# Kernel tuning notes

Measured on AMD Instinct MI355X. Metric: run time of the kernel, lower is better.

Reference implementation:

```python
import jax, jax.numpy as jnp
import numpy as np


def _l2norm(t, axis=-1, eps=1e-12):
    # matches torch F.normalize: x / max(||x||, eps)
    n = jnp.sqrt(jnp.sum(t * t, axis=axis, keepdims=True))
    return t / jnp.maximum(n, eps)


def setup_inputs() -> dict:
    key = jax.random.key(0)
    ks = jax.random.split(key, 5)
    B, N, C, H = 16, 4096, 768, 12
    x = jax.random.normal(ks[0], (B, N, C), dtype=jnp.float32)
    Wqkv = jax.random.normal(ks[1], (C, 3 * C), dtype=jnp.float32) * (C ** -0.5)
    bqkv = jax.random.normal(ks[2], (3 * C,), dtype=jnp.float32) * 0.02
    Wproj = jax.random.normal(ks[3], (C, C), dtype=jnp.float32) * (C ** -0.5)
    bproj = jax.random.normal(ks[4], (C,), dtype=jnp.float32) * 0.02
    temperature = jnp.ones((H, 1, 1), dtype=jnp.float32)
    return {"x": x, "Wqkv": Wqkv, "bqkv": bqkv, "Wproj": Wproj,
            "bproj": bproj, "temperature": temperature}


def reference(x, Wqkv, bqkv, Wproj, bproj, temperature):
    B, N, C = x.shape
    H = temperature.shape[0]
    Dh = C // H
    qkv = x @ Wqkv + bqkv                      # [B,N,3C]
    qkv = qkv.reshape(B, N, 3, H, Dh)
    # -> [3,B,H,Dh,N] (channels-as-tokens layout)
    qkv = jnp.transpose(qkv, (2, 0, 3, 4, 1))
    q, k, v = qkv[0], qkv[1], qkv[2]           # each [B,H,Dh,N]
    q = _l2norm(q, axis=-1)
    k = _l2norm(k, axis=-1)
    # cross-covariance over channels: [B,H,Dh,Dh]
    attn = jnp.einsum('bhdn,bhen->bhde', q, k) * temperature
    attn = jax.nn.softmax(attn, axis=-1)
    out = jnp.einsum('bhde,bhen->bhdn', attn, v)  # [B,H,Dh,N]
    out = jnp.transpose(out, (0, 3, 1, 2)).reshape(B, N, C)
    return out @ Wproj + bproj
```

## Files before the change

kernel.cpp:

```cpp
#include <hip/hip_runtime.h>

typedef __bf16 bf16x8 __attribute__((ext_vector_type(8)));
typedef float  f32x4  __attribute__((ext_vector_type(4)));
typedef unsigned short u16x8 __attribute__((ext_vector_type(8)));
typedef unsigned short u16x4 __attribute__((ext_vector_type(4)));

#define MFMA16(a, b, c) __builtin_amdgcn_mfma_f32_16x16x32_bf16((a), (b), (c), 0, 0, 0)

#define GLOAD16(g, l) __builtin_amdgcn_global_load_lds( \
    (const __attribute__((address_space(1))) void*)(g),  \
    (__attribute__((address_space(3))) void*)(l), 16, 0, 0)

__device__ __forceinline__ float bf2f(unsigned short u) {
    unsigned int x = ((unsigned int)u) << 16;
    return __builtin_bit_cast(float, x);
}
__device__ __forceinline__ unsigned short f2bf(float f) {
    unsigned int x = __builtin_bit_cast(unsigned int, f);
    x = x + 0x7FFFu + ((x >> 16) & 1u);
    return (unsigned short)(x >> 16);
}
__device__ __forceinline__ bool is_f32(const unsigned short* tf) { return tf[0] == 0; }
__device__ __forceinline__ float ldscal(const void* p, int i, bool f32m) {
    return f32m ? ((const float*)p)[i] : bf2f(((const unsigned short*)p)[i]);
}

__global__ __launch_bounds__(256)
void conv_x(const void* __restrict__ in, unsigned short* __restrict__ out,
            const unsigned short* __restrict__ tf)
{
    const bool f32m = is_f32(tf);
    const int n8 = 6291456;
    for (int i = blockIdx.x * 256 + threadIdx.x; i < n8; i += gridDim.x * 256) {
        u16x8 v;
        if (f32m) {
            const float* p = (const float*)in + (size_t)i * 8;
            f32x4 a = *(const f32x4*)p;
            f32x4 b = *(const f32x4*)(p + 4);
#pragma unroll
            for (int j = 0; j < 4; ++j) { v[j] = f2bf(a[j]); v[4 + j] = f2bf(b[j]); }
        } else {
            v = *(const u16x8*)((const unsigned short*)in + (size_t)i * 8);
        }
        *(u16x8*)&out[(size_t)i * 8] = v;
    }
}

__global__ __launch_bounds__(256)
void tr_conv(const void* __restrict__ in_, unsigned short* __restrict__ out,
             int R, int C, int istride, const unsigned short* __restrict__ tf)
{
    __shared__ unsigned short T[64 * 72];
    const bool f32m = is_f32(tf);
    const int nct = C >> 6;
    const int tx = blockIdx.x % nct;
    const int ty = blockIdx.x / nct;
    const int r0 = ty * 64, c0 = tx * 64;
    const int t = threadIdx.x;
#pragma unroll
    for (int s = 0; s < 2; ++s) {
        const int idx = t + s * 256;
        const int rr = idx >> 3;
        const int cc = (idx & 7) * 8;
        unsigned short v[8];
        if (f32m) {
            const float* inf = (const float*)in_;
            f32x4 a = *(const f32x4*)&inf[(size_t)(r0 + rr) * istride + c0 + cc];
            f32x4 b = *(const f32x4*)&inf[(size_t)(r0 + rr) * istride + c0 + cc + 4];
#pragma unroll
            for (int j = 0; j < 4; ++j) { v[j] = f2bf(a[j]); v[4 + j] = f2bf(b[j]); }
        } else {
            u16x8 a = *(const u16x8*)&((const unsigned short*)in_)[(size_t)(r0 + rr) * istride + c0 + cc];
#pragma unroll
            for (int j = 0; j < 8; ++j) v[j] = a[j];
        }
#pragma unroll
        for (int j = 0; j < 8; ++j) T[(cc + j) * 72 + rr] = v[j];
    }
    __syncthreads();
#pragma unroll
    for (int s = 0; s < 2; ++s) {
        const int idx = t + s * 256;
        const int cc = idx >> 3;
        const int rr = (idx & 7) * 8;
        u16x8 v = *(const u16x8*)&T[cc * 72 + rr];
        *(u16x8*)&out[(size_t)(c0 + cc) * R + r0 + rr] = v;
    }
}

__global__ __launch_bounds__(256)
void conv_wv(const void* __restrict__ Wqkv, unsigned short* __restrict__ Wv_bf,
             const unsigned short* __restrict__ tf)
{
    const bool f32m = is_f32(tf);
    const int t = blockIdx.x * 256 + threadIdx.x;
    const int c = t / 96;
    const int e0 = (t % 96) * 8;
    u16x8 v;
    if (f32m) {
        const float* p = (const float*)Wqkv + (size_t)c * 2304 + 1536 + e0;
        f32x4 a = *(const f32x4*)p;
        f32x4 b = *(const f32x4*)(p + 4);
#pragma unroll
        for (int j = 0; j < 4; ++j) { v[j] = f2bf(a[j]); v[4 + j] = f2bf(b[j]); }
    } else {
        v = *(const u16x8*)&((const unsigned short*)Wqkv)[(size_t)c * 2304 + 1536 + e0];
    }
    *(u16x8*)&Wv_bf[(size_t)c * 768 + e0] = v;
}

template<int MODE>
__global__ __launch_bounds__(512, 2)
void gemm256(const unsigned short* __restrict__ A,
             const unsigned short* __restrict__ BT,
             const void* __restrict__ bias,
             unsigned short* __restrict__ o0,
             unsigned short* __restrict__ o1,
             float* __restrict__ oF,
             const unsigned short* __restrict__ tf)
{
    constexpr int K = 768, NT = 12;
    constexpr int NB = (MODE == 0) ? 6 : 3;
    constexpr int LDSSZ = (MODE == 0) ? 135168 : 131072;
    __shared__ __align__(16) char SM[LDSSZ];
    unsigned short* lds = (unsigned short*)SM;

    const bool f32m = is_f32(tf);
    const int tid  = threadIdx.x;
    const int wave = tid >> 6;
    const int lane = tid & 63;
    const int wm   = wave >> 2;
    const int wn   = wave & 3;
    const int lr   = lane & 15;
    const int lq   = lane >> 4;

    const int per = gridDim.x >> 3;
    const int wg  = (blockIdx.x & 7) * per + (blockIdx.x >> 3);
    const int mt  = wg / NB;
    const int nt  = wg % NB;
    const size_t m0 = (size_t)mt * 256;
    const int n0 = nt * 256;

    const unsigned short* Bt = BT + ((MODE == 1) ? ((m0 >> 12) * (size_t)589824) : (size_t)0);

    f32x4 zero = {0.f, 0.f, 0.f, 0.f};
    f32x4 acc[8][4];
#pragma unroll
    for (int i = 0; i < 8; ++i)
#pragma unroll
        for (int j = 0; j < 4; ++j) acc[i][j] = zero;

    auto STAGE = [&](int t) {
        unsigned short* la_ = lds + (t & 1) * 32768;
        unsigned short* lb_ = la_ + 16384;
        const unsigned short* ga = A  + m0 * K + t * 64;
        const unsigned short* gb = Bt + (size_t)n0 * K + t * 64;
#pragma unroll
        for (int it = 0; it < 4; ++it) {
            const int c = it * 512 + tid;
            const int row = c >> 3;
            const int gs = (c & 7) ^ (row & 7);
            GLOAD16(ga + (size_t)row * K + gs * 8, la_ + c * 8);
        }
#pragma unroll
        for (int it = 0; it < 4; ++it) {
            const int c = it * 512 + tid;
            const int row = c >> 3;
            const int gs = (c & 7) ^ (row & 7);
            GLOAD16(gb + (size_t)row * K + gs * 8, lb_ + c * 8);
        }
    };

    STAGE(0);
    STAGE(1);

    bf16x8 af[4], bfr[4];

#define READ_B(ks) do { \
    _Pragma("unroll") for (int ni = 0; ni < 4; ++ni) { \
        const int row = wn * 64 + ni * 16 + lr; \
        bfr[ni] = *(const bf16x8*)(lb + row * 128 + ((((ks) * 4 + lq) ^ (row & 7)) << 4)); } } while (0)
#define READ_A(mh, ks) do { \
    _Pragma("unroll") for (int mi = 0; mi < 4; ++mi) { \
        const int row = wm * 128 + (mh) * 64 + mi * 16 + lr; \
        af[mi] = *(const bf16x8*)(la + row * 128 + ((((ks) * 4 + lq) ^ (row & 7)) << 4)); } } while (0)
#define MFMA_Q(mh) do { \
    _Pragma("unroll") for (int mi = 0; mi < 4; ++mi) \
    _Pragma("unroll") for (int ni = 0; ni < 4; ++ni) \
        acc[(mh) * 4 + mi][ni] = MFMA16(af[mi], bfr[ni], acc[(mh) * 4 + mi][ni]); } while (0)
#define PH_MID() do { \
    __builtin_amdgcn_sched_barrier(0); \
    __builtin_amdgcn_s_barrier(); \
    asm volatile("s_waitcnt lgkmcnt(0)" ::: "memory"); \
    __builtin_amdgcn_sched_barrier(0); } while (0)
#define PH_END() do { \
    __builtin_amdgcn_sched_barrier(0); \
    __builtin_amdgcn_s_barrier(); } while (0)

    for (int t = 0; t < NT; ++t) {
        if (t < NT - 1) asm volatile("s_waitcnt vmcnt(8)" ::: "memory");
        else            asm volatile("s_waitcnt vmcnt(0)" ::: "memory");
        __builtin_amdgcn_s_barrier();

        const char* la = (const char*)SM + (t & 1) * 65536;
        const char* lb = la + 32768;

        READ_B(0); READ_A(0, 0);
        PH_MID();
        __builtin_amdgcn_s_setprio(1); MFMA_Q(0); __builtin_amdgcn_s_setprio(0);
        PH_END();
        READ_A(1, 0);
        PH_MID();
        __builtin_amdgcn_s_setprio(1); MFMA_Q(1); __builtin_amdgcn_s_setprio(0);
        PH_END();
        READ_B(1); READ_A(0, 1);
        PH_MID();
        __builtin_amdgcn_s_setprio(1); MFMA_Q(0); __builtin_amdgcn_s_setprio(0);
        PH_END();
        READ_A(1, 1);
        asm volatile("s_waitcnt lgkmcnt(0)" ::: "memory");
        __builtin_amdgcn_sched_barrier(0);
        __builtin_amdgcn_s_barrier();
        if (t + 2 < NT) STAGE(t + 2);
        __builtin_amdgcn_s_setprio(1); MFMA_Q(1); __builtin_amdgcn_s_setprio(0);
    }
#undef READ_B
#undef READ_A
#undef MFMA_Q
#undef PH_MID
#undef PH_END

    float bb[4];
#pragma unroll
    for (int ni = 0; ni < 4; ++ni) {
        const int col = n0 + wn * 64 + ni * 16 + lr;
        if (MODE == 0)      bb[ni] = ldscal(bias, col, f32m);
        else if (MODE == 1) bb[ni] = ((const float*)bias)[(m0 >> 12) * 768 + col];
        else                bb[ni] = 0.f;
    }

    if (MODE == 1 || MODE == 2) {
#pragma unroll
        for (int mi = 0; mi < 8; ++mi)
#pragma unroll
            for (int ni = 0; ni < 4; ++ni)
#pragma unroll
                for (int r = 0; r < 4; ++r) {
                    const size_t row = m0 + (size_t)(wm * 128 + mi * 16 + lq * 4 + r);
                    const int col = n0 + wn * 64 + ni * 16 + lr;
                    const float val = acc[mi][ni][r] + bb[ni];
                    if (MODE == 2)      o0[row * 768 + col] = f2bf(val);
                    else if (f32m)      oF[row * 768 + col] = val;
                    else                o0[row * 768 + col] = f2bf(val);
                }
    } else {
        unsigned short* CTw = (unsigned short*)SM + wave * (64 * 132);
        const int cbase = (n0 < 768) ? n0 : (n0 - 768);
        unsigned short* dst = (n0 < 768) ? o0 : o1;
        const int h = (cbase >> 6) + wn;
        const size_t bh = (m0 >> 12) * 12 + h;
        const int tokbase = (int)(m0 & 4095) + wm * 128;
#pragma unroll
        for (int mi = 0; mi < 8; ++mi)
#pragma unroll
            for (int ni = 0; ni < 4; ++ni) {
                u16x4 pk;
#pragma unroll
                for (int r = 0; r < 4; ++r) pk[r] = f2bf(acc[mi][ni][r] + bb[ni]);
                *(u16x4*)&CTw[(ni * 16 + lr) * 132 + mi * 16 + lq * 4] = pk;
            }
#pragma unroll
        for (int rep = 0; rep < 16; ++rep) {
            const int d = rep * 4 + lq;
            u16x8 v = *(const u16x8*)&CTw[d * 132 + lr * 8];
            *(u16x8*)&dst[(bh * 64 + d) * 4096 + tokbase + lr * 8] = v;
        }
    }
}

__global__ __launch_bounds__(256)
void attn_sm(const unsigned short* __restrict__ qt,
             const unsigned short* __restrict__ ktb,
             const unsigned short* __restrict__ tf,
             unsigned short* __restrict__ attnT)
{
    __shared__ float S[64][64];
    __shared__ float nq[64];
    __shared__ float nk[64];
    const bool f32m = is_f32(tf);
    const int bh = blockIdx.x;
    const int h = bh % 12;
    const unsigned short* Q  = qt  + (size_t)bh * (64 * 4096);
    const unsigned short* Kp = ktb + (size_t)bh * (64 * 4096);
    const int tid = threadIdx.x;
    const int wave = tid >> 6;
    const int lane = tid & 63;
    if (tid < 64) { nq[tid] = 0.f; nk[tid] = 0.f; }

    f32x4 zero = {0.f, 0.f, 0.f, 0.f};
    f32x4 acc[4][4];
#pragma unroll
    for (int i = 0; i < 4; ++i)
#pragma unroll
        for (int j = 0; j < 4; ++j) acc[i][j] = zero;
    float sq[4] = {0.f, 0.f, 0.f, 0.f};
    float sk[4] = {0.f, 0.f, 0.f, 0.f};

    const int lr = lane & 15;
    const int lk = (lane >> 4) * 8;

    for (int it = 0; it < 32; ++it) {
        const int nb = (it * 4 + wave) * 32 + lk;
        u16x8 qa[4], ka[4];
#pragma unroll
        for (int mi = 0; mi < 4; ++mi)
            qa[mi] = *(const u16x8*)&Q[(size_t)(mi * 16 + lr) * 4096 + nb];
#pragma unroll
        for (int ni = 0; ni < 4; ++ni)
            ka[ni] = *(const u16x8*)&Kp[(size_t)(ni * 16 + lr) * 4096 + nb];
#pragma unroll
        for (int mi = 0; mi < 4; ++mi)
#pragma unroll
            for (int j = 0; j < 8; ++j) { float f = bf2f(qa[mi][j]); sq[mi] += f * f; }
#pragma unroll
        for (int ni = 0; ni < 4; ++ni)
#pragma unroll
            for (int j = 0; j < 8; ++j) { float f = bf2f(ka[ni][j]); sk[ni] += f * f; }
#pragma unroll
        for (int mi = 0; mi < 4; ++mi)
#pragma unroll
            for (int ni = 0; ni < 4; ++ni)
                acc[mi][ni] = MFMA16(__builtin_bit_cast(bf16x8, qa[mi]),
                                     __builtin_bit_cast(bf16x8, ka[ni]),
                                     acc[mi][ni]);
    }

    for (int ww = 0; ww < 4; ++ww) {
        if (wave == ww) {
#pragma unroll
            for (int mi = 0; mi < 4; ++mi)
#pragma unroll
                for (int ni = 0; ni < 4; ++ni)
#pragma unroll
                    for (int r = 0; r < 4; ++r) {
                        const int d = mi * 16 + (lane >> 4) * 4 + r;
                        const int e = ni * 16 + lr;
                        if (ww == 0) S[d][e] = acc[mi][ni][r];
                        else         S[d][e] += acc[mi][ni][r];
                    }
        }
        __syncthreads();
    }

#pragma unroll
    for (int mi = 0; mi < 4; ++mi) {
        float v = sq[mi];
        v += __shfl_xor(v, 16); v += __shfl_xor(v, 32);
        if (lane < 16) atomicAdd(&nq[mi * 16 + lane], v);
        float v2 = sk[mi];
        v2 += __shfl_xor(v2, 16); v2 += __shfl_xor(v2, 32);
        if (lane < 16) atomicAdd(&nk[mi * 16 + lane], v2);
    }
    __syncthreads();

    const int d  = tid >> 2;
    const int qq = tid & 3;
    const float tv = f32m ? ((const float*)tf)[h] : bf2f(tf[h]);
    const float qn = fmaxf(sqrtf(nq[d]), 1e-12f);
    float vals[16];
    float mx = -1e30f;
#pragma unroll
    for (int i = 0; i < 16; ++i) {
        const int e = qq * 16 + i;
        const float s = S[d][e] / (qn * fmaxf(sqrtf(nk[e]), 1e-12f)) * tv;
        vals[i] = s;
        mx = fmaxf(mx, s);
    }
    mx = fmaxf(mx, __shfl_xor(mx, 1));
    mx = fmaxf(mx, __shfl_xor(mx, 2));
    float sum = 0.f;
#pragma unroll
    for (int i = 0; i < 16; ++i) { vals[i] = __expf(vals[i] - mx); sum += vals[i]; }
    sum += __shfl_xor(sum, 1);
    sum += __shfl_xor(sum, 2);
    const float inv = 1.0f / sum;
#pragma unroll
    for (int i = 0; i < 16; ++i) {
        const int e = qq * 16 + i;
        attnT[(size_t)bh * 4096 + e * 64 + d] = f2bf(vals[i] * inv);
    }
}

__global__ __launch_bounds__(512)
void mb_build(const unsigned short* __restrict__ attnT,
              const unsigned short* __restrict__ WprojT,
              unsigned short* __restrict__ MbT)
{
    const int bh = blockIdx.x;
    const int b = bh / 12, h = bh % 12;
    const int tid = threadIdx.x;
    const int wave = tid >> 6;
    const int lane = tid & 63;
    const unsigned short* At = attnT + (size_t)bh * 4096;

    f32x4 zero = {0.f, 0.f, 0.f, 0.f};
    f32x4 acc[4][6];
#pragma unroll
    for (int i = 0; i < 4; ++i)
#pragma unroll
        for (int j = 0; j < 6; ++j) acc[i][j] = zero;

    const int lr  = lane & 15;
    const int lk8 = (lane >> 4) * 8;

#pragma unroll
    for (int ks = 0; ks < 2; ++ks) {
        bf16x8 af[4], bfr[6];
#pragma unroll
        for (int mi = 0; mi < 4; ++mi)
            af[mi] = *(const bf16x8*)&At[(mi * 16 + lr) * 64 + ks * 32 + lk8];
#pragma unroll
        for (int ni = 0; ni < 6; ++ni) {
            const int j = wave * 96 + ni * 16 + lr;
            bfr[ni] = *(const bf16x8*)&WprojT[(size_t)j * 768 + h * 64 + ks * 32 + lk8];
        }
#pragma unroll
        for (int mi = 0; mi < 4; ++mi)
#pragma unroll
            for (int ni = 0; ni < 6; ++ni)
                acc[mi][ni] = MFMA16(af[mi], bfr[ni], acc[mi][ni]);
    }

#pragma unroll
    for (int mi = 0; mi < 4; ++mi)
#pragma unroll
        for (int ni = 0; ni < 6; ++ni) {
            const int e = mi * 16 + (lane >> 4) * 4;
            const int j = wave * 96 + ni * 16 + lr;
            u16x4 pk;
#pragma unroll
            for (int r = 0; r < 4; ++r) pk[r] = f2bf(acc[mi][ni][r]);
            *(u16x4*)&MbT[(size_t)b * 589824 + (size_t)j * 768 + h * 64 + e] = pk;
        }
}

__global__ __launch_bounds__(256)
void beff_k(const unsigned short* __restrict__ MbT,
            const void* __restrict__ bqkv, const void* __restrict__ bp,
            float* __restrict__ beff, const unsigned short* __restrict__ tf)
{
    __shared__ float bv[768];
    const bool f32m = is_f32(tf);
    for (int i = threadIdx.x; i < 768; i += 256) bv[i] = ldscal(bqkv, 1536 + i, f32m);
    __syncthreads();
    const int t = blockIdx.x * 256 + threadIdx.x;
    const int b = t / 768, j = t % 768;
    float s = ldscal(bp, j, f32m);
    const unsigned short* row = MbT + (size_t)b * 589824 + (size_t)j * 768;
    for (int e8 = 0; e8 < 96; ++e8) {
        u16x8 m = *(const u16x8*)&row[e8 * 8];
#pragma unroll
        for (int jj = 0; jj < 8; ++jj) s += bf2f(m[jj]) * bv[e8 * 8 + jj];
    }
    beff[t] = s;
}

extern "C" void kernel_launch(void* const* d_in, const int* in_sizes, int n_in,
                              void* d_out, int out_size, void* d_ws, size_t ws_size,
                              hipStream_t stream)
{
    const void* x    = d_in[0];
    const void* Wqkv = d_in[1];
    const void* bqkv = d_in[2];
    const void* Wp   = d_in[3];
    const void* bp   = d_in[4];
    const unsigned short* tf = (const unsigned short*)d_in[5];

    char* w = (char*)d_ws;
    unsigned short* qt     = (unsigned short*)(w);
    unsigned short* PT     = (unsigned short*)(w);
    float*          beff   = (float*)(w + 18874368);
    unsigned short* ktb    = (unsigned short*)(w + 100663296);
    unsigned short* xb     = (unsigned short*)(w + 201326592);
    unsigned short* WqkT   = (unsigned short*)(w + 301989888);
    unsigned short* Wv_bf  = (unsigned short*)(w + 304349184);
    unsigned short* attnT  = (unsigned short*)(w + 305528832);
    unsigned short* MbT    = (unsigned short*)(w + 307101696);
    unsigned short* WprojT = (unsigned short*)(w + 325976064);

    conv_x <<<dim3(2048), dim3(256), 0, stream>>>(x, xb, tf);
    tr_conv<<<dim3(288),  dim3(256), 0, stream>>>(Wqkv, WqkT, 768, 1536, 2304, tf);
    conv_wv<<<dim3(288),  dim3(256), 0, stream>>>(Wqkv, Wv_bf, tf);
    tr_conv<<<dim3(144),  dim3(256), 0, stream>>>(Wp, WprojT, 768, 768, 768, tf);

    gemm256<0><<<dim3(1536), dim3(512), 0, stream>>>(xb, WqkT, bqkv, qt, ktb, nullptr, tf);
    attn_sm<<<dim3(192), dim3(256), 0, stream>>>(qt, ktb, tf, attnT);
    mb_build<<<dim3(192), dim3(512), 0, stream>>>(attnT, WprojT, MbT);
    gemm256<2><<<dim3(144), dim3(512), 0, stream>>>(MbT, Wv_bf, nullptr, PT, nullptr, nullptr, tf);
    beff_k<<<dim3(48), dim3(256), 0, stream>>>(MbT, bqkv, bp, beff, tf);
    gemm256<1><<<dim3(768), dim3(512), 0, stream>>>(xb, PT, beff,
        (unsigned short*)d_out, nullptr, (float*)d_out, tf);
}
```

Before: 494.9 us.

## Split GEMM K-tile staging into half-tiles and compute norms via MFMA Gram diagonal

The GEMM loads each 64-wide K tile as two 32-wide halves with a 4-way XOR swizzle on 64-byte rows. Those half-tile loads are interleaved across the four MFMA phases instead of being issued in one burst at the end of the iteration, which spreads global-to-LDS traffic and removes one barrier-heavy tail. Separately, the cross-covariance kernel replaces scalar sum-of-squares loops with extra MFMAs of Q and K against themselves and reads the squared norms off the diagonal. The finer-grained vmcnt accounting is easy to get wrong, and the self-MFMA adds matrix work in place of VALU work.

```diff
diff --git a/kernel.cpp b/kernel.cpp
--- a/kernel.cpp
+++ b/kernel.cpp
@@ -123,7 +123,6 @@
     constexpr int NB = (MODE == 0) ? 6 : 3;
     constexpr int LDSSZ = (MODE == 0) ? 135168 : 131072;
     __shared__ __align__(16) char SM[LDSSZ];
-    unsigned short* lds = (unsigned short*)SM;
 
     const bool f32m = is_f32(tf);
     const int tid  = threadIdx.x;
@@ -133,6 +132,7 @@
     const int wn   = wave & 3;
     const int lr   = lane & 15;
     const int lq   = lane >> 4;
+    const int sw16 = ((lq ^ (lr & 3)) << 4);
 
     const int per = gridDim.x >> 3;
     const int wg  = (blockIdx.x & 7) * per + (blockIdx.x >> 3);
@@ -150,40 +150,30 @@
 #pragma unroll
         for (int j = 0; j < 4; ++j) acc[i][j] = zero;
 
-    auto STAGE = [&](int t) {
-        unsigned short* la_ = lds + (t & 1) * 32768;
-        unsigned short* lb_ = la_ + 16384;
-        const unsigned short* ga = A  + m0 * K + t * 64;
-        const unsigned short* gb = Bt + (size_t)n0 * K + t * 64;
-#pragma unroll
-        for (int it = 0; it < 4; ++it) {
-            const int c = it * 512 + tid;
-            const int row = c >> 3;
-            const int gs = (c & 7) ^ (row & 7);
-            GLOAD16(ga + (size_t)row * K + gs * 8, la_ + c * 8);
-        }
-#pragma unroll
-        for (int it = 0; it < 4; ++it) {
-            const int c = it * 512 + tid;
-            const int row = c >> 3;
-            const int gs = (c & 7) ^ (row & 7);
-            GLOAD16(gb + (size_t)row * K + gs * 8, lb_ + c * 8);
+    auto STAGE_EV = [&](int mat, int kh, int t) {
+        const unsigned short* g = mat ? (Bt + (size_t)n0 * K) : (A + m0 * K);
+        char* dst = SM + (t & 1) * 65536 + mat * 32768 + kh * 16384;
+#pragma unroll
+        for (int ev = 0; ev < 2; ++ev) {
+            const int c = ev * 512 + tid;
+            const int row = c >> 2;
+            const int sg  = (c & 3) ^ (row & 3);
+            GLOAD16(g + (size_t)row * K + t * 64 + kh * 32 + sg * 8, dst + c * 16);
         }
     };
 
-    STAGE(0);
-    STAGE(1);
+    STAGE_EV(0, 0, 0); STAGE_EV(1, 0, 0);
+    STAGE_EV(0, 1, 0); STAGE_EV(1, 1, 0);
+    STAGE_EV(0, 0, 1); STAGE_EV(1, 0, 1);
 
     bf16x8 af[4], bfr[4];
 
 #define READ_B(ks) do { \
-    _Pragma("unroll") for (int ni = 0; ni < 4; ++ni) { \
-        const int row = wn * 64 + ni * 16 + lr; \
-        bfr[ni] = *(const bf16x8*)(lb + row * 128 + ((((ks) * 4 + lq) ^ (row & 7)) << 4)); } } while (0)
+    _Pragma("unroll") for (int ni = 0; ni < 4; ++ni) \
+        bfr[ni] = *(const bf16x8*)(lb + (ks) * 16384 + (wn * 64 + ni * 16 + lr) * 64 + sw16); } while (0)
 #define READ_A(mh, ks) do { \
-    _Pragma("unroll") for (int mi = 0; mi < 4; ++mi) { \
-        const int row = wm * 128 + (mh) * 64 + mi * 16 + lr; \
-        af[mi] = *(const bf16x8*)(la + row * 128 + ((((ks) * 4 + lq) ^ (row & 7)) << 4)); } } while (0)
+    _Pragma("unroll") for (int mi = 0; mi < 4; ++mi) \
+        af[mi] = *(const bf16x8*)(la + (ks) * 16384 + (wm * 128 + (mh) * 64 + mi * 16 + lr) * 64 + sw16); } while (0)
 #define MFMA_Q(mh) do { \
     _Pragma("unroll") for (int mi = 0; mi < 4; ++mi) \
     _Pragma("unroll") for (int ni = 0; ni < 4; ++ni) \
@@ -198,37 +188,48 @@
     __builtin_amdgcn_s_barrier(); } while (0)
 
     for (int t = 0; t < NT; ++t) {
-        if (t < NT - 1) asm volatile("s_waitcnt vmcnt(8)" ::: "memory");
-        else            asm volatile("s_waitcnt vmcnt(0)" ::: "memory");
-        __builtin_amdgcn_s_barrier();
-
         const char* la = (const char*)SM + (t & 1) * 65536;
         const char* lb = la + 32768;
 
+        if (t < NT - 1) asm volatile("s_waitcnt vmcnt(8)" ::: "memory");
+        else            asm volatile("s_waitcnt vmcnt(4)" ::: "memory");
+        __builtin_amdgcn_s_barrier();
+        __builtin_amdgcn_sched_barrier(0);
+
         READ_B(0); READ_A(0, 0);
+        if (t + 1 < NT) STAGE_EV(0, 1, t + 1);
         PH_MID();
         __builtin_amdgcn_s_setprio(1); MFMA_Q(0); __builtin_amdgcn_s_setprio(0);
         PH_END();
+
         READ_A(1, 0);
+        if (t + 1 < NT) STAGE_EV(1, 1, t + 1);
+        if (t < NT - 1) asm volatile("s_waitcnt vmcnt(8)" ::: "memory");
+        else            asm volatile("s_waitcnt vmcnt(0)" ::: "memory");
         PH_MID();
         __builtin_amdgcn_s_setprio(1); MFMA_Q(1); __builtin_amdgcn_s_setprio(0);
         PH_END();
+
         READ_B(1); READ_A(0, 1);
+        if (t + 2 < NT) STAGE_EV(0, 0, t + 2);
         PH_MID();
         __builtin_amdgcn_s_setprio(1); MFMA_Q(0); __builtin_amdgcn_s_setprio(0);
         PH_END();
+
         READ_A(1, 1);
-        asm volatile("s_waitcnt lgkmcnt(0)" ::: "memory");
-        __builtin_amdgcn_sched_barrier(0);
-        __builtin_amdgcn_s_barrier();
-        if (t + 2 < NT) STAGE(t + 2);
+        if (t + 2 < NT) STAGE_EV(1, 0, t + 2);
+        PH_MID();
         __builtin_amdgcn_s_setprio(1); MFMA_Q(1); __builtin_amdgcn_s_setprio(0);
+        PH_END();
     }
 #undef READ_B
 #undef READ_A
 #undef MFMA_Q
 #undef PH_MID
 #undef PH_END
+
+    asm volatile("s_waitcnt lgkmcnt(0)" ::: "memory");
+    __builtin_amdgcn_s_barrier();
 
     float bb[4];
 #pragma unroll
@@ -303,11 +304,13 @@
     for (int i = 0; i < 4; ++i)
 #pragma unroll
         for (int j = 0; j < 4; ++j) acc[i][j] = zero;
-    float sq[4] = {0.f, 0.f, 0.f, 0.f};
-    float sk[4] = {0.f, 0.f, 0.f, 0.f};
+    f32x4 gq[4], gk[4];
+#pragma unroll
+    for (int i = 0; i < 4; ++i) { gq[i] = zero; gk[i] = zero; }
 
     const int lr = lane & 15;
-    const int lk = (lane >> 4) * 8;
+    const int lq = lane >> 4;
+    const int lk = lq * 8;
 
     for (int it = 0; it < 32; ++it) {
         const int nb = (it * 4 + wave) * 32 + lk;
@@ -319,13 +322,12 @@
         for (int ni = 0; ni < 4; ++ni)
             ka[ni] = *(const u16x8*)&Kp[(size_t)(ni * 16 + lr) * 4096 + nb];
 #pragma unroll
-        for (int mi = 0; mi < 4; ++mi)
-#pragma unroll
-            for (int j = 0; j < 8; ++j) { float f = bf2f(qa[mi][j]); sq[mi] += f * f; }
-#pragma unroll
-        for (int ni = 0; ni < 4; ++ni)
-#pragma unroll
-            for (int j = 0; j < 8; ++j) { float f = bf2f(ka[ni][j]); sk[ni] += f * f; }
+        for (int mi = 0; mi < 4; ++mi) {
+            gq[mi] = MFMA16(__builtin_bit_cast(bf16x8, qa[mi]),
+                            __builtin_bit_cast(bf16x8, qa[mi]), gq[mi]);
+            gk[mi] = MFMA16(__builtin_bit_cast(bf16x8, ka[mi]),
+                            __builtin_bit_cast(bf16x8, ka[mi]), gk[mi]);
+        }
 #pragma unroll
         for (int mi = 0; mi < 4; ++mi)
 #pragma unroll
@@ -343,7 +345,7 @@
                 for (int ni = 0; ni < 4; ++ni)
 #pragma unroll
                     for (int r = 0; r < 4; ++r) {
-                        const int d = mi * 16 + (lane >> 4) * 4 + r;
+                        const int d = mi * 16 + lq * 4 + r;
                         const int e = ni * 16 + lr;
                         if (ww == 0) S[d][e] = acc[mi][ni][r];
                         else         S[d][e] += acc[mi][ni][r];
@@ -352,14 +354,15 @@
         __syncthreads();
     }
 
-#pragma unroll
-    for (int mi = 0; mi < 4; ++mi) {
-        float v = sq[mi];
-        v += __shfl_xor(v, 16); v += __shfl_xor(v, 32);
-        if (lane < 16) atomicAdd(&nq[mi * 16 + lane], v);
-        float v2 = sk[mi];
-        v2 += __shfl_xor(v2, 16); v2 += __shfl_xor(v2, 32);
-        if (lane < 16) atomicAdd(&nk[mi * 16 + lane], v2);
+    {
+        const int rdiag = lr - lq * 4;
+        if (rdiag >= 0 && rdiag < 4) {
+#pragma unroll
+            for (int mi = 0; mi < 4; ++mi) {
+                atomicAdd(&nq[mi * 16 + lr], gq[mi][rdiag]);
+                atomicAdd(&nk[mi * 16 + lr], gk[mi][rdiag]);
+            }
+        }
     }
     __syncthreads();
 
```

Result: faster. 473.2 us (-4.4%).
